# Kernel optimization log

Hardware: AMD Instinct MI355X
Metric: run time of the kernel (lower is better)

## Reference

```python
import jax, jax.numpy as jnp
import numpy as np

N_NODES = 5000
N_EDGES = 80000
IN_DIM = 128
HID_DIM = 128
OUT_DIM = 64
NUM_HEADS = 1
BATCH = 8
NEG_SLOPE = 0.2  # DGL GATConv default leaky_relu negative_slope


def setup_inputs() -> dict:
    key = jax.random.key(0)
    ks = jax.random.split(key, 12)
    x = jax.random.normal(ks[0], (BATCH, N_NODES, IN_DIM), dtype=jnp.float32)
    src = jax.random.randint(ks[1], (N_EDGES,), 0, N_NODES)
    dst = jax.random.randint(ks[2], (N_EDGES,), 0, N_NODES)
    # layer1 params (fc has no bias in DGL GATConv; output bias present by default)
    s1 = 1.0 / np.sqrt(IN_DIM)
    W1 = jax.random.normal(ks[3], (IN_DIM, NUM_HEADS * HID_DIM), dtype=jnp.float32) * s1
    al1 = jax.random.normal(ks[4], (NUM_HEADS, HID_DIM), dtype=jnp.float32) * 0.1
    ar1 = jax.random.normal(ks[5], (NUM_HEADS, HID_DIM), dtype=jnp.float32) * 0.1
    b1 = jnp.zeros((NUM_HEADS * HID_DIM,), dtype=jnp.float32)
    # layer2 params
    s2 = 1.0 / np.sqrt(NUM_HEADS * HID_DIM)
    W2 = jax.random.normal(ks[6], (NUM_HEADS * HID_DIM, NUM_HEADS * OUT_DIM), dtype=jnp.float32) * s2
    al2 = jax.random.normal(ks[7], (NUM_HEADS, OUT_DIM), dtype=jnp.float32) * 0.1
    ar2 = jax.random.normal(ks[8], (NUM_HEADS, OUT_DIM), dtype=jnp.float32) * 0.1
    b2 = jnp.zeros((NUM_HEADS * OUT_DIM,), dtype=jnp.float32)
    return {"x": x, "W1": W1, "al1": al1, "ar1": ar1, "b1": b1,
            "W2": W2, "al2": al2, "ar2": ar2, "b2": b2,
            "src": src, "dst": dst}


def gat_layer(x, W, al, ar, b, src, dst, n_nodes):
    """DGL GATConv. x:[B,N,Din] W:[Din,H*F] al/ar:[H,F] b:[H*F] -> [B,N,H,F]."""
    B = x.shape[0]
    H, F = al.shape
    z = (x @ W).reshape(B, n_nodes, H, F)                 # [B,N,H,F]
    el = jnp.einsum('bnhf,hf->bnh', z, al)                # src-side attn term
    er = jnp.einsum('bnhf,hf->bnh', z, ar)                # dst-side attn term
    e = jax.nn.leaky_relu(el[:, src] + er[:, dst], NEG_SLOPE)  # [B,E,H]
    e = jnp.moveaxis(e, 1, 0)                             # [E,B,H]  edge-major for segment ops
    emax = jax.ops.segment_max(e, dst, num_segments=n_nodes)   # [N,B,H]
    ex = jnp.exp(e - emax[dst])
    denom = jax.ops.segment_sum(ex, dst, num_segments=n_nodes)  # [N,B,H]
    alpha = ex / denom[dst]                               # edge softmax over incoming edges
    zs = jnp.moveaxis(z[:, src], 1, 0)                    # [E,B,H,F] gathered source feats
    out = jax.ops.segment_sum(alpha[..., None] * zs, dst, num_segments=n_nodes)  # [N,B,H,F]
    return jnp.moveaxis(out, 0, 1) + b.reshape(1, 1, H, F)


def reference(x, W1, al1, ar1, b1, W2, al2, ar2, b2, src, dst):
    n_nodes = x.shape[1]
    h = gat_layer(x, W1, al1, ar1, b1, src, dst, n_nodes)  # [B,N,H,hid]
    B, N, H, Fh = h.shape
    h = h.reshape(B, N, H * Fh)                            # concat heads (H=1)
    o = gat_layer(h, W2, al2, ar2, b2, src, dst, n_nodes)  # [B,N,H,out]
    o = o.reshape(B * N, -1)                               # squeeze: [B*N, out]
    return jax.nn.softmax(o, axis=-1)
```

## Files before the change

### kernel.cpp

```cpp
#include <hip/hip_runtime.h>
#include <hip/hip_bf16.h>

#define N_NODES 5000
#define N_EDGES 80000
#define HID_DIM 128
#define OUT_DIM 64
#define BATCH 8
#define M_ROWS 40000
#define NEG_SLOPE 0.2f
#define BUCKET 96


typedef unsigned short ushort_t;
typedef unsigned int uint_t;
typedef __attribute__((ext_vector_type(8))) short short8;
typedef __attribute__((ext_vector_type(4))) float f32x4;

__device__ __forceinline__ float bf16_to_f32(ushort_t u) {
  return __uint_as_float(((uint_t)u) << 16);
}
__device__ __forceinline__ ushort_t f32_to_bf16(float f) {
  uint_t u = __float_as_uint(f);
  return (ushort_t)((u + 0x7FFF + ((u >> 16) & 1)) >> 16);
}

struct __attribute__((aligned(8))) us4 { ushort_t x, y, z, w; };

__global__ __launch_bounds__(256) void zero_pack_kernel(const float* __restrict__ W1,
                                                        const float* __restrict__ W2,
                                                        int* __restrict__ cnt,
                                                        ushort_t* __restrict__ Bp1,
                                                        ushort_t* __restrict__ Bp2) {
  int bid = blockIdx.x;
  if (bid < 20) {
    int i = bid * 256 + threadIdx.x;
    if (i < N_NODES) cnt[i] = 0;
    return;
  }
  int gid = (bid - 20) * 256 + threadIdx.x;
  if (gid >= 3072) return;
  const float* W; ushort_t* Bp; int NC, idx;
  if (gid < 2048) { W = W1; Bp = Bp1; NC = 128; idx = gid; }
  else            { W = W2; Bp = Bp2; NC = 64;  idx = gid - 2048; }
  int l = idx & 63, tt = idx >> 6;
  int T = NC / 16;
  int kc = tt / T, t = tt % T;
  int col = t * 16 + (l & 15);
  int krow = kc * 32 + (l >> 4) * 8;
  short8 vv;
#pragma unroll
  for (int j = 0; j < 8; j++) vv[j] = (short)f32_to_bf16(W[(size_t)(krow + j) * NC + col]);
  *(short8*)(Bp + (size_t)idx * 8) = vv;
}

template <int NC, bool A_F32, bool C_BF16, bool SCATTER>
__global__ __launch_bounds__(256) void gemm_mfma(const void* __restrict__ A,
                                                 const ushort_t* __restrict__ Bp,
                                                 void* __restrict__ C,
                                                 const float* __restrict__ al,
                                                 const float* __restrict__ ar,
                                                 float* __restrict__ el,
                                                 float* __restrict__ er,
                                                 const int* __restrict__ e_src,
                                                 const int* __restrict__ e_dst,
                                                 int* __restrict__ cnt,
                                                 int* __restrict__ srcs) {
  if (SCATTER) {
    int tid = threadIdx.x;
    if (tid < 128) {
      int i = blockIdx.x * 128 + tid;
      int d = e_dst[i];
      int pos = atomicAdd(&cnt[d], 1);
      if (pos < BUCKET) srcs[d * BUCKET + pos] = e_src[i];
    }
  }
  constexpr int T = NC / 16;
  int wave = threadIdx.x >> 6, lane = threadIdx.x & 63;
  int q = lane >> 4, m = lane & 15;
  int r0 = blockIdx.x * 64 + wave * 16;
  f32x4 acc[T];
#pragma unroll
  for (int t = 0; t < T; t++)
#pragma unroll
    for (int i = 0; i < 4; i++) acc[t][i] = 0.f;

  const short8* Bp8 = (const short8*)Bp;
  size_t arow = (size_t)(r0 + m) * 128;
#pragma unroll
  for (int kc = 0; kc < 4; kc++) {
    short8 af;
    if (A_F32) {
      const float* Ap = (const float*)A + arow + kc * 32 + q * 8;
      float4 v0 = *(const float4*)Ap;
      float4 v1 = *(const float4*)(Ap + 4);
      af[0] = (short)f32_to_bf16(v0.x); af[1] = (short)f32_to_bf16(v0.y);
      af[2] = (short)f32_to_bf16(v0.z); af[3] = (short)f32_to_bf16(v0.w);
      af[4] = (short)f32_to_bf16(v1.x); af[5] = (short)f32_to_bf16(v1.y);
      af[6] = (short)f32_to_bf16(v1.z); af[7] = (short)f32_to_bf16(v1.w);
    } else {
      const ushort_t* Ap = (const ushort_t*)A + arow + kc * 32 + q * 8;
      us4 a0 = *(const us4*)Ap;
      us4 a1 = *(const us4*)(Ap + 4);
      af[0] = (short)a0.x; af[1] = (short)a0.y; af[2] = (short)a0.z; af[3] = (short)a0.w;
      af[4] = (short)a1.x; af[5] = (short)a1.y; af[6] = (short)a1.z; af[7] = (short)a1.w;
    }
#pragma unroll
    for (int t = 0; t < T; t++) {
      short8 bf = Bp8[(kc * T + t) * 64 + lane];
      acc[t] = __builtin_amdgcn_mfma_f32_16x16x32_bf16(af, bf, acc[t], 0, 0, 0);
    }
  }
  float sl[4] = {0.f, 0.f, 0.f, 0.f}, sr[4] = {0.f, 0.f, 0.f, 0.f};
#pragma unroll
  for (int t = 0; t < T; t++) {
    float alv = al[t * 16 + m];
    float arv = ar[t * 16 + m];
#pragma unroll
    for (int i = 0; i < 4; i++) { sl[i] += acc[t][i] * alv; sr[i] += acc[t][i] * arv; }
  }
#pragma unroll
  for (int o = 1; o < 16; o <<= 1) {
#pragma unroll
    for (int i = 0; i < 4; i++) {
      sl[i] += __shfl_xor(sl[i], o, 64);
      sr[i] += __shfl_xor(sr[i], o, 64);
    }
  }
  if (m == 0) {
#pragma unroll
    for (int i = 0; i < 4; i++) {
      el[r0 + q * 4 + i] = sl[i];
      er[r0 + q * 4 + i] = sr[i];
    }
  }
#pragma unroll
  for (int t = 0; t < T; t++)
#pragma unroll
    for (int i = 0; i < 4; i++) {
      size_t off = (size_t)(r0 + q * 4 + i) * NC + t * 16 + m;
      if (C_BF16) ((ushort_t*)C)[off] = f32_to_bf16(acc[t][i]);
      else        ((float*)C)[off] = acc[t][i];
    }
}

template <int F, bool FINAL>
__global__ __launch_bounds__(256) void agg_kernel(const void* __restrict__ z,
                                                  const float* __restrict__ el,
                                                  const float* __restrict__ er,
                                                  const float* __restrict__ bias,
                                                  const int* __restrict__ cnt,
                                                  const int* __restrict__ srcs,
                                                  void* __restrict__ outp) {
  int id = (threadIdx.x >> 6) * gridDim.x + blockIdx.x;
  int lane = threadIdx.x & 63;
  int g = lane >> 4, l16 = lane & 15;
  int b = id & 7, n = id >> 3;
  int deg = cnt[n]; if (deg > BUCKET) deg = BUCKET;
  int off0 = n * BUCKET;
  int rbase = b * N_NODES;
  float er_n = er[rbase + n];

  constexpr int J = (F == 128) ? 8 : 4;
  float acc[J];
#pragma unroll
  for (int j = 0; j < J; j++) acc[j] = 0.f;
  float lsum = 0.f;

  for (int c = 0; c < deg; c += 64) {
    int j = c + lane;
    int s_my = 0;
    float w_my = 0.f;
    if (j < deg) {
      s_my = srcs[off0 + j];
      float e = el[rbase + s_my] + er_n;
      e = e > 0.f ? e : NEG_SLOPE * e;
      w_my = __expf(e);
      lsum += w_my;
    }
    int cl = deg - c; if (cl > 64) cl = 64;
    for (int k4 = 0; k4 < cl; k4 += 4) {
      int e_idx = k4 + g;
      float wk = __shfl(w_my, e_idx, 64);
      int sk = __shfl(s_my, e_idx, 64);
      if (F == 128) {
        uint4 zw = *(const uint4*)((const ushort_t*)z + (size_t)(rbase + sk) * F + l16 * 8);
        acc[0] += wk * bf16_to_f32((ushort_t)(zw.x & 0xFFFF));
        acc[1] += wk * bf16_to_f32((ushort_t)(zw.x >> 16));
        acc[2] += wk * bf16_to_f32((ushort_t)(zw.y & 0xFFFF));
        acc[3] += wk * bf16_to_f32((ushort_t)(zw.y >> 16));
        acc[4] += wk * bf16_to_f32((ushort_t)(zw.z & 0xFFFF));
        acc[5] += wk * bf16_to_f32((ushort_t)(zw.z >> 16));
        acc[6] += wk * bf16_to_f32((ushort_t)(zw.w & 0xFFFF));
        acc[7] += wk * bf16_to_f32((ushort_t)(zw.w >> 16));
      } else {
        uint2 zw = *(const uint2*)((const ushort_t*)z + (size_t)(rbase + sk) * F + l16 * 4);
        acc[0] += wk * bf16_to_f32((ushort_t)(zw.x & 0xFFFF));
        acc[1] += wk * bf16_to_f32((ushort_t)(zw.x >> 16));
        acc[2] += wk * bf16_to_f32((ushort_t)(zw.y & 0xFFFF));
        acc[3] += wk * bf16_to_f32((ushort_t)(zw.y >> 16));
      }
    }
  }
#pragma unroll
  for (int j = 0; j < J; j++) {
    acc[j] += __shfl_xor(acc[j], 16, 64);
    acc[j] += __shfl_xor(acc[j], 32, 64);
  }
  float sum = lsum;
#pragma unroll
  for (int o = 32; o; o >>= 1) sum += __shfl_xor(sum, o, 64);
  float inv = (deg > 0) ? 1.f / sum : 0.f;

  if (!FINAL) {
    if (g == 0) {
      uint_t pk[4];
#pragma unroll
      for (int p = 0; p < 4; p++) {
        float o0 = acc[2 * p] * inv + bias[l16 * 8 + 2 * p];
        float o1 = acc[2 * p + 1] * inv + bias[l16 * 8 + 2 * p + 1];
        pk[p] = (uint_t)f32_to_bf16(o0) | ((uint_t)f32_to_bf16(o1) << 16);
      }
      *(uint4*)((ushort_t*)outp + (size_t)(rbase + n) * F + l16 * 8) =
          make_uint4(pk[0], pk[1], pk[2], pk[3]);
    }
  } else {
    float o[4];
#pragma unroll
    for (int j = 0; j < 4; j++) o[j] = acc[j] * inv + bias[l16 * 4 + j];
    float mm = fmaxf(fmaxf(o[0], o[1]), fmaxf(o[2], o[3]));
#pragma unroll
    for (int d = 1; d < 16; d <<= 1) mm = fmaxf(mm, __shfl_xor(mm, d, 64));
    float p0 = __expf(o[0] - mm), p1 = __expf(o[1] - mm);
    float p2 = __expf(o[2] - mm), p3 = __expf(o[3] - mm);
    float ss = p0 + p1 + p2 + p3;
#pragma unroll
    for (int d = 1; d < 16; d <<= 1) ss += __shfl_xor(ss, d, 64);
    if (g == 0) {
      float issv = 1.f / ss;
      *(float4*)((float*)outp + (size_t)(rbase + n) * F + l16 * 4) =
          make_float4(p0 * issv, p1 * issv, p2 * issv, p3 * issv);
    }
  }
}

extern "C" void kernel_launch(void* const* d_in, const int* in_sizes, int n_in,
                              void* d_out, int out_size, void* d_ws, size_t ws_size,
                              hipStream_t stream) {
  const float* x   = (const float*)d_in[0];
  const float* W1  = (const float*)d_in[1];
  const float* al1 = (const float*)d_in[2];
  const float* ar1 = (const float*)d_in[3];
  const float* b1  = (const float*)d_in[4];
  const float* W2  = (const float*)d_in[5];
  const float* al2 = (const float*)d_in[6];
  const float* ar2 = (const float*)d_in[7];
  const float* b2  = (const float*)d_in[8];
  const int* src = (const int*)d_in[9];
  const int* dst = (const int*)d_in[10];

  char* base = (char*)d_ws;
  ushort_t* Bp1 = (ushort_t*)base;
  ushort_t* Bp2 = Bp1 + 16384;
  ushort_t* z1  = (ushort_t*)(base + 49152);
  ushort_t* z2  = (ushort_t*)(base + 49152);
  ushort_t* h   = (ushort_t*)(base + 10289152);
  float* el1    = (float*)(base + 20529152);
  float* er1    = el1 + M_ROWS;
  float* el2    = er1 + M_ROWS;
  float* er2    = el2 + M_ROWS;
  int* cnt      = (int*)(base + 20529152 + 640000);
  int* srcs     = cnt + N_NODES;

  zero_pack_kernel<<<32, 256, 0, stream>>>(W1, W2, cnt, Bp1, Bp2);

  gemm_mfma<HID_DIM, true, true, true><<<M_ROWS / 64, 256, 0, stream>>>(
      x, Bp1, z1, al1, ar1, el1, er1, src, dst, cnt, srcs);

  agg_kernel<HID_DIM, false><<<M_ROWS / 4, 256, 0, stream>>>(z1, el1, er1, b1, cnt, srcs, h);

  gemm_mfma<OUT_DIM, false, true, false><<<M_ROWS / 64, 256, 0, stream>>>(
      h, Bp2, z2, al2, ar2, el2, er2, nullptr, nullptr, nullptr, nullptr);

  agg_kernel<OUT_DIM, true><<<M_ROWS / 4, 256, 0, stream>>>(z2, el2, er2, b2, cnt, srcs, d_out);
}
```

Baseline: 153.1 us.

## Fuse GEMM and aggregation stages into one persistent kernel with grid barriers

Replaces four separate launches (two GEMMs, two aggregations) with a single persistent kernel of 512 blocks that loops over tiles and node-batch units, separated by software grid barriers built on atomic counters. The edge scatter into per-node buckets is folded into the first phase. This aims to remove kernel launch gaps and tail effects between stages. In exchange it depends on all 512 blocks being co-resident for the spin barriers to avoid deadlock, and the barrier spins add their own synchronization cost.

```diff
diff --git a/kernel.cpp b/kernel.cpp
--- a/kernel.cpp
+++ b/kernel.cpp
@@ -9,6 +9,7 @@
 #define M_ROWS 40000
 #define NEG_SLOPE 0.2f
 #define BUCKET 96
+#define GRID_BLOCKS 512
 
 
 typedef unsigned short ushort_t;
@@ -26,12 +27,26 @@
 
 struct __attribute__((aligned(8))) us4 { ushort_t x, y, z, w; };
 
-__global__ __launch_bounds__(256) void zero_pack_kernel(const float* __restrict__ W1,
-                                                        const float* __restrict__ W2,
-                                                        int* __restrict__ cnt,
-                                                        ushort_t* __restrict__ Bp1,
-                                                        ushort_t* __restrict__ Bp2) {
+__device__ __forceinline__ void grid_barrier(int* __restrict__ bar) {
+  __syncthreads();
+  if (threadIdx.x == 0) {
+    __threadfence();
+    __hip_atomic_fetch_add(bar, 1, __ATOMIC_RELAXED, __HIP_MEMORY_SCOPE_AGENT);
+    while (__hip_atomic_load(bar, __ATOMIC_RELAXED, __HIP_MEMORY_SCOPE_AGENT) < GRID_BLOCKS)
+      __builtin_amdgcn_s_sleep(2);
+    __threadfence();
+  }
+  __syncthreads();
+}
+
+__global__ __launch_bounds__(256) void setup_kernel(const float* __restrict__ W1,
+                                                    const float* __restrict__ W2,
+                                                    int* __restrict__ cnt,
+                                                    ushort_t* __restrict__ Bp1,
+                                                    ushort_t* __restrict__ Bp2,
+                                                    int* __restrict__ bar) {
   int bid = blockIdx.x;
+  if (bid == 0 && threadIdx.x < 3) bar[threadIdx.x * 32] = 0;
   if (bid < 20) {
     int i = bid * 256 + threadIdx.x;
     if (i < N_NODES) cnt[i] = 0;
@@ -53,31 +68,19 @@
   *(short8*)(Bp + (size_t)idx * 8) = vv;
 }
 
-template <int NC, bool A_F32, bool C_BF16, bool SCATTER>
-__global__ __launch_bounds__(256) void gemm_mfma(const void* __restrict__ A,
-                                                 const ushort_t* __restrict__ Bp,
-                                                 void* __restrict__ C,
-                                                 const float* __restrict__ al,
-                                                 const float* __restrict__ ar,
-                                                 float* __restrict__ el,
-                                                 float* __restrict__ er,
-                                                 const int* __restrict__ e_src,
-                                                 const int* __restrict__ e_dst,
-                                                 int* __restrict__ cnt,
-                                                 int* __restrict__ srcs) {
-  if (SCATTER) {
-    int tid = threadIdx.x;
-    if (tid < 128) {
-      int i = blockIdx.x * 128 + tid;
-      int d = e_dst[i];
-      int pos = atomicAdd(&cnt[d], 1);
-      if (pos < BUCKET) srcs[d * BUCKET + pos] = e_src[i];
-    }
-  }
+template <int NC, bool A_F32, bool C_BF16>
+__device__ __forceinline__ void gemm_tile(const void* __restrict__ A,
+                                          const ushort_t* __restrict__ Bp,
+                                          void* __restrict__ C,
+                                          const float* __restrict__ al,
+                                          const float* __restrict__ ar,
+                                          float* __restrict__ el,
+                                          float* __restrict__ er,
+                                          int tile) {
   constexpr int T = NC / 16;
   int wave = threadIdx.x >> 6, lane = threadIdx.x & 63;
   int q = lane >> 4, m = lane & 15;
-  int r0 = blockIdx.x * 64 + wave * 16;
+  int r0 = tile * 64 + wave * 16;
   f32x4 acc[T];
 #pragma unroll
   for (int t = 0; t < T; t++)
@@ -144,14 +147,14 @@
 }
 
 template <int F, bool FINAL>
-__global__ __launch_bounds__(256) void agg_kernel(const void* __restrict__ z,
-                                                  const float* __restrict__ el,
-                                                  const float* __restrict__ er,
-                                                  const float* __restrict__ bias,
-                                                  const int* __restrict__ cnt,
-                                                  const int* __restrict__ srcs,
-                                                  void* __restrict__ outp) {
-  int id = (threadIdx.x >> 6) * gridDim.x + blockIdx.x;
+__device__ __forceinline__ void agg_unit(const void* __restrict__ z,
+                                         const float* __restrict__ el,
+                                         const float* __restrict__ er,
+                                         const float* __restrict__ bias,
+                                         const int* __restrict__ cnt,
+                                         const int* __restrict__ srcs,
+                                         void* __restrict__ outp,
+                                         int id) {
   int lane = threadIdx.x & 63;
   int g = lane >> 4, l16 = lane & 15;
   int b = id & 7, n = id >> 3;
@@ -243,6 +246,61 @@
   }
 }
 
+__global__ __launch_bounds__(256, 3) void fused_gat(const float* __restrict__ x,
+                                                    const float* __restrict__ al1,
+                                                    const float* __restrict__ ar1,
+                                                    const float* __restrict__ b1,
+                                                    const float* __restrict__ al2,
+                                                    const float* __restrict__ ar2,
+                                                    const float* __restrict__ b2,
+                                                    const int* __restrict__ e_src,
+                                                    const int* __restrict__ e_dst,
+                                                    char* __restrict__ ws,
+                                                    float* __restrict__ outp) {
+  ushort_t* Bp1 = (ushort_t*)ws;
+  ushort_t* Bp2 = Bp1 + 16384;
+  ushort_t* z1  = (ushort_t*)(ws + 49152);
+  ushort_t* z2  = (ushort_t*)(ws + 49152);
+  ushort_t* h   = (ushort_t*)(ws + 10289152);
+  float* el1    = (float*)(ws + 20529152);
+  float* er1    = el1 + M_ROWS;
+  float* el2    = er1 + M_ROWS;
+  float* er2    = el2 + M_ROWS;
+  int* cnt      = (int*)(ws + 20529152 + 640000);
+  int* srcs     = cnt + N_NODES;
+  int* bar      = (int*)(ws + 23200000);
+
+  int bid = blockIdx.x, tid = threadIdx.x;
+  int wave = tid >> 6;
+
+  {
+    int i = bid * 256 + tid;
+    if (i < N_EDGES) {
+      int d = e_dst[i];
+      int pos = atomicAdd(&cnt[d], 1);
+      if (pos < BUCKET) srcs[d * BUCKET + pos] = e_src[i];
+    }
+  }
+  for (int tile = bid; tile < M_ROWS / 64; tile += GRID_BLOCKS)
+    gemm_tile<HID_DIM, true, true>(x, Bp1, z1, al1, ar1, el1, er1, tile);
+  grid_barrier(bar);
+
+  for (int j = 0; j < 20; j++) {
+    int id = j * (GRID_BLOCKS * 4) + wave * GRID_BLOCKS + bid;
+    if (id < M_ROWS) agg_unit<HID_DIM, false>(z1, el1, er1, b1, cnt, srcs, h, id);
+  }
+  grid_barrier(bar + 32);
+
+  for (int tile = bid; tile < M_ROWS / 64; tile += GRID_BLOCKS)
+    gemm_tile<OUT_DIM, false, true>(h, Bp2, z2, al2, ar2, el2, er2, tile);
+  grid_barrier(bar + 64);
+
+  for (int j = 0; j < 20; j++) {
+    int id = j * (GRID_BLOCKS * 4) + wave * GRID_BLOCKS + bid;
+    if (id < M_ROWS) agg_unit<OUT_DIM, true>(z2, el2, er2, b2, cnt, srcs, outp, id);
+  }
+}
+
 extern "C" void kernel_launch(void* const* d_in, const int* in_sizes, int n_in,
                               void* d_out, int out_size, void* d_ws, size_t ws_size,
                               hipStream_t stream) {
@@ -257,29 +315,15 @@
   const float* b2  = (const float*)d_in[8];
   const int* src = (const int*)d_in[9];
   const int* dst = (const int*)d_in[10];
-
-  char* base = (char*)d_ws;
-  ushort_t* Bp1 = (ushort_t*)base;
+  char* ws = (char*)d_ws;
+
+  ushort_t* Bp1 = (ushort_t*)ws;
   ushort_t* Bp2 = Bp1 + 16384;
-  ushort_t* z1  = (ushort_t*)(base + 49152);
-  ushort_t* z2  = (ushort_t*)(base + 49152);
-  ushort_t* h   = (ushort_t*)(base + 10289152);
-  float* el1    = (float*)(base + 20529152);
-  float* er1    = el1 + M_ROWS;
-  float* el2    = er1 + M_ROWS;
-  float* er2    = el2 + M_ROWS;
-  int* cnt      = (int*)(base + 20529152 + 640000);
-  int* srcs     = cnt + N_NODES;
-
-  zero_pack_kernel<<<32, 256, 0, stream>>>(W1, W2, cnt, Bp1, Bp2);
-
-  gemm_mfma<HID_DIM, true, true, true><<<M_ROWS / 64, 256, 0, stream>>>(
-      x, Bp1, z1, al1, ar1, el1, er1, src, dst, cnt, srcs);
-
-  agg_kernel<HID_DIM, false><<<M_ROWS / 4, 256, 0, stream>>>(z1, el1, er1, b1, cnt, srcs, h);
-
-  gemm_mfma<OUT_DIM, false, true, false><<<M_ROWS / 64, 256, 0, stream>>>(
-      h, Bp2, z2, al2, ar2, el2, er2, nullptr, nullptr, nullptr, nullptr);
-
-  agg_kernel<OUT_DIM, true><<<M_ROWS / 4, 256, 0, stream>>>(z2, el2, er2, b2, cnt, srcs, d_out);
-}
+  int* cnt = (int*)(ws + 20529152 + 640000);
+  int* bar = (int*)(ws + 23200000);
+
+  setup_kernel<<<32, 256, 0, stream>>>(W1, W2, cnt, Bp1, Bp2, bar);
+
+  fused_gat<<<GRID_BLOCKS, 256, 0, stream>>>(x, al1, ar1, b1, al2, ar2, b2,
+                                             src, dst, ws, (float*)d_out);
+}
```

New measurement: 394.2 us. +157.4%, slower.
